# Kernel optimization log

Measured on AMD Instinct MI355X. Metric: run time of the kernel, lower is better.

The kernel has to match this reference:

```python
import jax, jax.numpy as jnp
import numpy as np

N_GRAPHS = 500
EPS = 1e-5


def setup_inputs() -> dict:
    key = jax.random.key(0)
    ks = jax.random.split(key, 10)
    N, H, OUT, E = 50000, 96, 10, 800000
    s = 1.0 / np.sqrt(H)
    x = jax.random.normal(ks[0], (N, H), jnp.float32)
    edge_index = jax.random.randint(ks[1], (2, E), 0, N, jnp.int32)
    batch = jnp.sort(jax.random.randint(ks[2], (N,), 0, N_GRAPHS, jnp.int32))
    convW = jax.random.normal(ks[3], (6, H, H), jnp.float32) * s
    convB = jnp.zeros((6, H), jnp.float32)
    bnG = jnp.ones((5, H), jnp.float32)
    bnB = jnp.zeros((5, H), jnp.float32)
    W1 = jax.random.normal(ks[4], (H, H), jnp.float32) * s
    b1 = jnp.zeros((H,), jnp.float32)
    g1 = jnp.ones((H,), jnp.float32)
    be1 = jnp.zeros((H,), jnp.float32)
    W2 = jax.random.normal(ks[5], (H, H), jnp.float32) * s
    b2 = jnp.zeros((H,), jnp.float32)
    W3 = jax.random.normal(ks[6], (H, OUT), jnp.float32) * s
    b3 = jnp.zeros((OUT,), jnp.float32)
    return dict(x=x, edge_index=edge_index, batch=batch, convW=convW, convB=convB,
                bnG=bnG, bnB=bnB, W1=W1, b1=b1, g1=g1, be1=be1, W2=W2, b2=b2, W3=W3, b3=b3)


def _batchnorm(h, g, b):
    # track_running_stats=False -> always use batch statistics (biased var)
    mu = h.mean(axis=0)
    v = jnp.mean((h - mu) ** 2, axis=0)
    return (h - mu) * jax.lax.rsqrt(v + EPS) * g + b


def reference(x, edge_index, batch, convW, convB, bnG, bnB, W1, b1, g1, be1, W2, b2, W3, b3):
    N = x.shape[0]
    src, dst = edge_index[0], edge_index[1]
    # GCN symmetric normalization with self-loops: A_hat = D^-1/2 (A+I) D^-1/2
    deg = jnp.zeros((N,), x.dtype).at[dst].add(1.0) + 1.0  # +1 for self loop
    dinv = jax.lax.rsqrt(deg)
    ew = dinv[src] * dinv[dst]            # [E] edge weights
    self_w = dinv * dinv                   # [N] self-loop weights (1/deg)

    def gcn_conv(h, W, b):
        h = h @ W
        agg = jnp.zeros_like(h).at[dst].add(ew[:, None] * h[src])
        return agg + self_w[:, None] * h + b

    # PyG BasicGNN: layers 0..4 -> conv+norm+relu+dropout; layer 5 -> conv only.
    # Dropout is identity in eval mode.
    for i in range(6):
        x = gcn_conv(x, convW[i], convB[i])
        if i < 5:
            x = jax.nn.relu(_batchnorm(x, bnG[i], bnB[i]))

    # global_mean_pool over `batch`
    cnt = jax.ops.segment_sum(jnp.ones((N,), x.dtype), batch, num_segments=N_GRAPHS)
    pooled = jax.ops.segment_sum(x, batch, num_segments=N_GRAPHS) / jnp.maximum(cnt, 1.0)[:, None]

    # prediction head: Linear -> BN -> ReLU -> (Dropout) -> Linear -> ReLU -> Linear
    h = jax.nn.relu(_batchnorm(pooled @ W1 + b1, g1, be1))
    h = jax.nn.relu(h @ W2 + b2)
    return h @ W3 + b3
```

## Files before the change

### kernel.cpp

```cpp
#include <hip/hip_runtime.h>
#include <hip/hip_fp16.h>

#define HF 96
#define C4 24
#define CH 12
#define NGRAPHS 500
#define POOL_SL 8
#define MMROWS 64
#define ATP 104
#define EPS 1e-5f

typedef _Float16 half8 __attribute__((ext_vector_type(8)));
typedef float f32x4 __attribute__((ext_vector_type(4)));

__device__ __forceinline__ float4 h4tof4(uint2 u) {
    __half2 a = *(__half2*)&u.x;
    __half2 b = *(__half2*)&u.y;
    float2 fa = __half22float2(a);
    float2 fb = __half22float2(b);
    return make_float4(fa.x, fa.y, fb.x, fb.y);
}


__global__ void count_kernel(const int* __restrict__ dst, int E, int* __restrict__ cnt) {
    int stride = gridDim.x * blockDim.x;
    for (int i = blockIdx.x * blockDim.x + threadIdx.x; i < E; i += stride)
        atomicAdd(&cnt[dst[i]], 1);
}

__global__ void node_init_kernel(const int* __restrict__ cnt, int N,
                                 float* __restrict__ dinv, float* __restrict__ selfw) {
    int stride = gridDim.x * blockDim.x;
    for (int i = blockIdx.x * blockDim.x + threadIdx.x; i < N; i += stride) {
        float d = (float)(cnt[i] + 1);
        dinv[i] = 1.0f / sqrtf(d);
        selfw[i] = 1.0f / d;
    }
}

__global__ void scan1_kernel(const int* __restrict__ cnt, int N, int* __restrict__ bsum) {
    __shared__ int s[256];
    int t = threadIdx.x;
    int i = blockIdx.x * 256 + t;
    s[t] = (i < N) ? cnt[i] : 0;
    __syncthreads();
    for (int off = 128; off; off >>= 1) {
        if (t < off) s[t] += s[t + off];
        __syncthreads();
    }
    if (t == 0) bsum[blockIdx.x] = s[0];
}

__global__ void scan2_kernel(const int* __restrict__ bsum, int NB,
                             int* __restrict__ boff, int* __restrict__ row_ptr, int N) {
    __shared__ int s[256];
    int t = threadIdx.x;
    int v = (t < NB) ? bsum[t] : 0;
    s[t] = v;
    __syncthreads();
    for (int off = 1; off < 256; off <<= 1) {
        int u = (t >= off) ? s[t - off] : 0;
        __syncthreads();
        s[t] += u;
        __syncthreads();
    }
    if (t < NB) boff[t] = s[t] - v;
    if (t == 255) row_ptr[N] = s[255];
}

__global__ void scan3_kernel(int* __restrict__ cnt, int N, const int* __restrict__ boff,
                             int* __restrict__ row_ptr) {
    __shared__ int s[256];
    int t = threadIdx.x;
    int i = blockIdx.x * 256 + t;
    int v = (i < N) ? cnt[i] : 0;
    s[t] = v;
    __syncthreads();
    for (int off = 1; off < 256; off <<= 1) {
        int u = (t >= off) ? s[t - off] : 0;
        __syncthreads();
        s[t] += u;
        __syncthreads();
    }
    if (i < N) {
        row_ptr[i] = boff[blockIdx.x] + s[t] - v;
        cnt[i] = 0;
    }
}

__global__ void scatter_kernel(const int* __restrict__ src, const int* __restrict__ dst, int E,
                               const int* __restrict__ row_ptr, int* __restrict__ cnt,
                               const float* __restrict__ dinv,
                               int2* __restrict__ csr) {
    int stride = gridDim.x * blockDim.x;
    for (int i = blockIdx.x * blockDim.x + threadIdx.x; i < E; i += stride) {
        int d = dst[i], s = src[i];
        int p = row_ptr[d] + atomicAdd(&cnt[d], 1);
        float w = dinv[s] * dinv[d];
        csr[p] = make_int2(s, __float_as_int(w));
    }
}


__global__ __launch_bounds__(256) void
matmul_kernel(const float* __restrict__ in, const float* __restrict__ W,
              _Float16* __restrict__ out, int N, int applyBN,
              const double* __restrict__ bnsum,
              const float* __restrict__ bnG, const float* __restrict__ bnB) {
    __shared__ _Float16 At[MMROWS][ATP];
    __shared__ _Float16 Wt[HF][ATP];
    __shared__ float sAl[HF], sBe[HF];
    int t = threadIdx.x;
    int n0 = blockIdx.x * MMROWS;
    int rows = N - n0; if (rows > MMROWS) rows = MMROWS;

    if (t < HF) {
        float a = 1.f, b = 0.f;
        if (applyBN) {
            double invN = 1.0 / (double)N;
            double mu = bnsum[t] * invN;
            double var = bnsum[HF + t] * invN - mu * mu;
            float v = fmaxf((float)var, 0.f) + EPS;
            a = bnG[t] / sqrtf(v);
            b = bnB[t] - (float)mu * a;
        }
        sAl[t] = a; sBe[t] = b;
    }
    __syncthreads();

#pragma unroll
    for (int j = 0; j < 6; ++j) {
        int gi = t + j * 256;
        int r = gi / C4, c4 = gi % C4;
        if (r < rows) {
            float4 v = ((const float4*)(in + (size_t)(n0 + r) * HF))[c4];
            int k = c4 * 4;
            if (applyBN) {
                v.x = fmaxf(fmaf(v.x, sAl[k + 0], sBe[k + 0]), 0.f);
                v.y = fmaxf(fmaf(v.y, sAl[k + 1], sBe[k + 1]), 0.f);
                v.z = fmaxf(fmaf(v.z, sAl[k + 2], sBe[k + 2]), 0.f);
                v.w = fmaxf(fmaf(v.w, sAl[k + 3], sBe[k + 3]), 0.f);
            }
            At[r][k + 0] = (_Float16)v.x; At[r][k + 1] = (_Float16)v.y;
            At[r][k + 2] = (_Float16)v.z; At[r][k + 3] = (_Float16)v.w;
        }
    }
#pragma unroll
    for (int j = 0; j < 9; ++j) {
        int gi = t + j * 256;
        int k = gi / C4, f4 = gi % C4;
        float4 v = ((const float4*)(W + (size_t)k * HF))[f4];
        int f = f4 * 4;
        Wt[f + 0][k] = (_Float16)v.x; Wt[f + 1][k] = (_Float16)v.y;
        Wt[f + 2][k] = (_Float16)v.z; Wt[f + 3][k] = (_Float16)v.w;
    }
    __syncthreads();

    int w = t >> 6;
    int lane = t & 63;
    int arow = w * 16 + (lane & 15);
    int k0 = (lane >> 4) * 8;
    f32x4 acc[6];
#pragma unroll
    for (int ft = 0; ft < 6; ++ft) acc[ft] = (f32x4){0.f, 0.f, 0.f, 0.f};
#pragma unroll
    for (int ks = 0; ks < 3; ++ks) {
        half8 a = *(const half8*)&At[arow][ks * 32 + k0];
#pragma unroll
        for (int ft = 0; ft < 6; ++ft) {
            half8 b = *(const half8*)&Wt[ft * 16 + (lane & 15)][ks * 32 + k0];
            acc[ft] = __builtin_amdgcn_mfma_f32_16x16x32_f16(a, b, acc[ft], 0, 0, 0);
        }
    }
    int fcol = lane & 15;
#pragma unroll
    for (int ft = 0; ft < 6; ++ft) {
#pragma unroll
        for (int j = 0; j < 4; ++j) {
            int r = w * 16 + (lane >> 4) * 4 + j;
            if (r < rows)
                out[(size_t)(n0 + r) * HF + ft * 16 + fcol] = (_Float16)acc[ft][j];
        }
    }
}


__global__ __launch_bounds__(256) void
agg_kernel(const __half* __restrict__ Hb, float* __restrict__ out,
           const int* __restrict__ row_ptr, const int2* __restrict__ csr,
           const float* __restrict__ selfw, const float* __restrict__ convB,
           int N, double* __restrict__ bnsum) {
    __shared__ float sred[2 * HF];
    bool stats = (bnsum != nullptr);
    for (int i = threadIdx.x; i < 2 * HF; i += blockDim.x) sred[i] = 0.f;
    __syncthreads();
    const uint4* h4p = (const uint4*)Hb;
    int total = N * CH;
    int stride = gridDim.x * blockDim.x;
    for (int idx = blockIdx.x * blockDim.x + threadIdx.x; idx < total; idx += stride) {
        int n = idx / CH, c = idx % CH;
        const uint4* hp = h4p + c;
        int p0 = row_ptr[n], p1 = row_ptr[n + 1];
        float sw = selfw[n];
        uint4 hraw = hp[(size_t)n * CH];
        float4 hlo = h4tof4(make_uint2(hraw.x, hraw.y));
        float4 hhi = h4tof4(make_uint2(hraw.z, hraw.w));
        float4 blo = ((const float4*)convB)[2 * c];
        float4 bhi = ((const float4*)convB)[2 * c + 1];
        float4 alo, ahi;
        alo.x = fmaf(sw, hlo.x, blo.x); alo.y = fmaf(sw, hlo.y, blo.y);
        alo.z = fmaf(sw, hlo.z, blo.z); alo.w = fmaf(sw, hlo.w, blo.w);
        ahi.x = fmaf(sw, hhi.x, bhi.x); ahi.y = fmaf(sw, hhi.y, bhi.y);
        ahi.z = fmaf(sw, hhi.z, bhi.z); ahi.w = fmaf(sw, hhi.w, bhi.w);
#define EDGE(EV, RV) { \
            float w = __int_as_float(EV.y); \
            float4 vlo = h4tof4(make_uint2(RV.x, RV.y)); \
            float4 vhi = h4tof4(make_uint2(RV.z, RV.w)); \
            alo.x = fmaf(w, vlo.x, alo.x); alo.y = fmaf(w, vlo.y, alo.y); \
            alo.z = fmaf(w, vlo.z, alo.z); alo.w = fmaf(w, vlo.w, alo.w); \
            ahi.x = fmaf(w, vhi.x, ahi.x); ahi.y = fmaf(w, vhi.y, ahi.y); \
            ahi.z = fmaf(w, vhi.z, ahi.z); ahi.w = fmaf(w, vhi.w, ahi.w); }
        int p = p0;
        for (; p + 4 <= p1; p += 4) {
            int2 e0 = csr[p], e1 = csr[p + 1], e2 = csr[p + 2], e3 = csr[p + 3];
            uint4 g0 = hp[(size_t)e0.x * CH];
            uint4 g1 = hp[(size_t)e1.x * CH];
            uint4 g2 = hp[(size_t)e2.x * CH];
            uint4 g3 = hp[(size_t)e3.x * CH];
            EDGE(e0, g0) EDGE(e1, g1) EDGE(e2, g2) EDGE(e3, g3)
        }
        for (; p < p1; ++p) {
            int2 e = csr[p];
            uint4 g = hp[(size_t)e.x * CH];
            EDGE(e, g)
        }
#undef EDGE
        ((float4*)out)[2 * idx]     = alo;
        ((float4*)out)[2 * idx + 1] = ahi;
        if (stats) {
            int f = 8 * c;
            atomicAdd(&sred[f + 0], alo.x); atomicAdd(&sred[f + 1], alo.y);
            atomicAdd(&sred[f + 2], alo.z); atomicAdd(&sred[f + 3], alo.w);
            atomicAdd(&sred[f + 4], ahi.x); atomicAdd(&sred[f + 5], ahi.y);
            atomicAdd(&sred[f + 6], ahi.z); atomicAdd(&sred[f + 7], ahi.w);
            atomicAdd(&sred[HF + f + 0], alo.x * alo.x); atomicAdd(&sred[HF + f + 1], alo.y * alo.y);
            atomicAdd(&sred[HF + f + 2], alo.z * alo.z); atomicAdd(&sred[HF + f + 3], alo.w * alo.w);
            atomicAdd(&sred[HF + f + 4], ahi.x * ahi.x); atomicAdd(&sred[HF + f + 5], ahi.y * ahi.y);
            atomicAdd(&sred[HF + f + 6], ahi.z * ahi.z); atomicAdd(&sred[HF + f + 7], ahi.w * ahi.w);
        }
    }
    if (stats) {
        __syncthreads();
        for (int i = threadIdx.x; i < 2 * HF; i += blockDim.x)
            atomicAdd(&bnsum[i], (double)sred[i]);
    }
}


__global__ __launch_bounds__(256) void
pool_kernel(const float* __restrict__ xin, const int* __restrict__ batch, int N,
            float* __restrict__ pooled) {
    int idx = blockIdx.x * blockDim.x + threadIdx.x;
    int total = NGRAPHS * POOL_SL * C4;
    if (idx >= total) return;
    int c = idx % C4;
    int q = (idx / C4) % POOL_SL;
    int g = idx / (C4 * POOL_SL);
    int lo = 0, hi = N;
    while (lo < hi) { int m = (lo + hi) >> 1; if (batch[m] < g) lo = m + 1; else hi = m; }
    int s0 = lo;
    lo = s0; hi = N;
    while (lo < hi) { int m = (lo + hi) >> 1; if (batch[m] < g + 1) lo = m + 1; else hi = m; }
    int len = lo - s0;
    int n0 = s0 + (len * q) / POOL_SL;
    int n1 = s0 + (len * (q + 1)) / POOL_SL;
    const float4* x4 = (const float4*)xin;
    float4 acc = make_float4(0.f, 0.f, 0.f, 0.f);
    for (int n = n0; n < n1; ++n) {
        float4 v0 = x4[(size_t)n * C4 + c];
        acc.x += v0.x; acc.y += v0.y; acc.z += v0.z; acc.w += v0.w;
    }
    atomicAdd(&pooled[g * HF + 4 * c + 0], acc.x);
    atomicAdd(&pooled[g * HF + 4 * c + 1], acc.y);
    atomicAdd(&pooled[g * HF + 4 * c + 2], acc.z);
    atomicAdd(&pooled[g * HF + 4 * c + 3], acc.w);
}

__global__ __launch_bounds__(128) void
head1_kernel(const float* __restrict__ pooled, const int* __restrict__ batch, int N,
             const float* __restrict__ W1, const float* __restrict__ b1,
             float* __restrict__ tmp1, double* __restrict__ bnsum) {
    __shared__ float row[HF];
    int g = blockIdx.x;
    int lo = 0, hi = N;
    while (lo < hi) { int m = (lo + hi) >> 1; if (batch[m] < g) lo = m + 1; else hi = m; }
    int s0 = lo;
    lo = s0; hi = N;
    while (lo < hi) { int m = (lo + hi) >> 1; if (batch[m] < g + 1) lo = m + 1; else hi = m; }
    int len = lo - s0;
    float inv = 1.0f / fmaxf((float)len, 1.0f);
    int f = threadIdx.x;
    if (f < HF) row[f] = pooled[g * HF + f] * inv;
    __syncthreads();
    if (f < HF) {
        float acc = b1[f];
        for (int k = 0; k < HF; ++k) acc = fmaf(row[k], W1[k * HF + f], acc);
        tmp1[g * HF + f] = acc;
        atomicAdd(&bnsum[f], (double)acc);
        atomicAdd(&bnsum[HF + f], (double)(acc * acc));
    }
}

__global__ __launch_bounds__(128) void
head23_kernel(const float* __restrict__ tmp1, const double* __restrict__ bnsum,
              const float* __restrict__ g1, const float* __restrict__ be1,
              const float* __restrict__ W2, const float* __restrict__ b2,
              const float* __restrict__ W3, const float* __restrict__ b3,
              float* __restrict__ out) {
    __shared__ float row[HF], row2[HF];
    int g = blockIdx.x;
    int f = threadIdx.x;
    if (f < HF) {
        double mu = bnsum[f] / (double)NGRAPHS;
        double var = bnsum[HF + f] / (double)NGRAPHS - mu * mu;
        float v = fmaxf((float)var, 0.f) + EPS;
        float a = g1[f] / sqrtf(v);
        float bb = be1[f] - (float)mu * a;
        row[f] = fmaxf(fmaf(tmp1[g * HF + f], a, bb), 0.f);
    }
    __syncthreads();
    if (f < HF) {
        float acc = b2[f];
        for (int k = 0; k < HF; ++k) acc = fmaf(row[k], W2[k * HF + f], acc);
        row2[f] = fmaxf(acc, 0.f);
    }
    __syncthreads();
    if (f < 10) {
        float acc = b3[f];
        for (int k = 0; k < HF; ++k) acc = fmaf(row2[k], W3[k * 10 + f], acc);
        out[g * 10 + f] = acc;
    }
}


extern "C" void kernel_launch(void* const* d_in, const int* in_sizes, int n_in,
                              void* d_out, int out_size, void* d_ws, size_t ws_size,
                              hipStream_t stream) {
    (void)n_in; (void)out_size; (void)ws_size;
    const float* x     = (const float*)d_in[0];
    const int*   ei    = (const int*)d_in[1];
    const int*   batch = (const int*)d_in[2];
    const float* convW = (const float*)d_in[3];
    const float* convB = (const float*)d_in[4];
    const float* bnG   = (const float*)d_in[5];
    const float* bnB   = (const float*)d_in[6];
    const float* W1    = (const float*)d_in[7];
    const float* b1    = (const float*)d_in[8];
    const float* g1    = (const float*)d_in[9];
    const float* be1   = (const float*)d_in[10];
    const float* W2    = (const float*)d_in[11];
    const float* b2    = (const float*)d_in[12];
    const float* W3    = (const float*)d_in[13];
    const float* b3    = (const float*)d_in[14];
    float* outp = (float*)d_out;

    int N = in_sizes[0] / HF;
    int E = in_sizes[1] / 2;
    int NB = (N + 255) / 256;
    const int* src  = ei;
    const int* dstp = ei + E;

    char* ws = (char*)d_ws;
    size_t off = 0;
    auto alloc = [&](size_t bytes) -> char* {
        char* p = ws + off;
        off += (bytes + 255) & ~(size_t)255;
        return p;
    };
    _Float16* Hb   = (_Float16*)alloc((size_t)N * HF * 2);
    float* Ob      = (float*)alloc((size_t)N * HF * 4);
    int2*  csr     = (int2*)alloc((size_t)E * 8);
    int*   row_ptr = (int*)alloc((size_t)(N + 1) * 4);
    float* dinv    = (float*)alloc((size_t)N * 4);
    float* selfw   = (float*)alloc((size_t)N * 4);
    int*   bsum    = (int*)alloc((size_t)NB * 4);
    int*   boff    = (int*)alloc((size_t)NB * 4);
    float* tmp1    = (float*)alloc((size_t)NGRAPHS * HF * 4);
    char* zstart   = ws + off;
    int*    cnt    = (int*)alloc((size_t)N * 4);
    double* bns    = (double*)alloc(6 * 2 * HF * 8);
    float*  pooled = (float*)alloc((size_t)NGRAPHS * HF * 4);
    size_t zbytes  = (size_t)((ws + off) - zstart);

    hipMemsetAsync(zstart, 0, zbytes, stream);

    count_kernel<<<1024, 256, 0, stream>>>(dstp, E, cnt);
    node_init_kernel<<<(N + 255) / 256, 256, 0, stream>>>(cnt, N, dinv, selfw);
    scan1_kernel<<<NB, 256, 0, stream>>>(cnt, N, bsum);
    scan2_kernel<<<1, 256, 0, stream>>>(bsum, NB, boff, row_ptr, N);
    scan3_kernel<<<NB, 256, 0, stream>>>(cnt, N, boff, row_ptr);
    scatter_kernel<<<1024, 256, 0, stream>>>(src, dstp, E, row_ptr, cnt, dinv, csr);

    int agg_grid = (N * CH + 255) / 256;
    int mm_grid = (N + MMROWS - 1) / MMROWS;
    const float* cur = x;
    for (int i = 0; i < 6; ++i) {
        matmul_kernel<<<mm_grid, 256, 0, stream>>>(
            cur, convW + (size_t)i * HF * HF, Hb, N,
            (i > 0) ? 1 : 0,
            (i > 0) ? bns + (size_t)(i - 1) * 2 * HF : nullptr,
            (i > 0) ? bnG + (size_t)(i - 1) * HF : nullptr,
            (i > 0) ? bnB + (size_t)(i - 1) * HF : nullptr);
        agg_kernel<<<agg_grid, 256, 0, stream>>>(
            (const __half*)Hb, Ob, row_ptr, csr, selfw,
            convB + (size_t)i * HF, N,
            (i < 5) ? bns + (size_t)i * 2 * HF : nullptr);
        cur = Ob;
    }

    int pool_grid = (NGRAPHS * POOL_SL * C4 + 255) / 256;
    pool_kernel<<<pool_grid, 256, 0, stream>>>(Ob, batch, N, pooled);
    head1_kernel<<<NGRAPHS, 128, 0, stream>>>(pooled, batch, N, W1, b1, tmp1, bns + 5 * 2 * HF);
    head23_kernel<<<NGRAPHS, 128, 0, stream>>>(tmp1, bns + 5 * 2 * HF, g1, be1, W2, b2, W3, b3, outp);
}
```

Measured before the change: 750.5 us.

## Store aggregation outputs in fp16 and fuse pooling with head layer

Aggregation now writes its output in fp16 instead of fp32, so the next matmul reads half the bytes. The matmul gains an fp16 input path that applies BN and ReLU after converting each loaded row to float. Pooling and the first head linear are merged into one per-graph kernel that reduces through shared memory, removing the global atomics. The degree/dinv init is folded into the scan3 kernel. This saves memory traffic and launches, but rounding pre-BN activations to fp16 adds precision risk, and the BN statistics are still taken from the fp32 accumulators before rounding.

```diff
diff --git a/kernel.cpp b/kernel.cpp
--- a/kernel.cpp
+++ b/kernel.cpp
@@ -5,9 +5,9 @@
 #define C4 24
 #define CH 12
 #define NGRAPHS 500
-#define POOL_SL 8
 #define MMROWS 64
 #define ATP 104
+#define PSL 20
 #define EPS 1e-5f
 
 typedef _Float16 half8 __attribute__((ext_vector_type(8)));
@@ -20,22 +20,17 @@
     float2 fb = __half22float2(b);
     return make_float4(fa.x, fa.y, fb.x, fb.y);
 }
+__device__ __forceinline__ uint2 f4toh4(float4 v) {
+    __half2 a = __floats2half2_rn(v.x, v.y);
+    __half2 b = __floats2half2_rn(v.z, v.w);
+    return make_uint2(*(unsigned int*)&a, *(unsigned int*)&b);
+}
 
 
 __global__ void count_kernel(const int* __restrict__ dst, int E, int* __restrict__ cnt) {
     int stride = gridDim.x * blockDim.x;
     for (int i = blockIdx.x * blockDim.x + threadIdx.x; i < E; i += stride)
         atomicAdd(&cnt[dst[i]], 1);
-}
-
-__global__ void node_init_kernel(const int* __restrict__ cnt, int N,
-                                 float* __restrict__ dinv, float* __restrict__ selfw) {
-    int stride = gridDim.x * blockDim.x;
-    for (int i = blockIdx.x * blockDim.x + threadIdx.x; i < N; i += stride) {
-        float d = (float)(cnt[i] + 1);
-        dinv[i] = 1.0f / sqrtf(d);
-        selfw[i] = 1.0f / d;
-    }
 }
 
 __global__ void scan1_kernel(const int* __restrict__ cnt, int N, int* __restrict__ bsum) {
@@ -69,7 +64,8 @@
 }
 
 __global__ void scan3_kernel(int* __restrict__ cnt, int N, const int* __restrict__ boff,
-                             int* __restrict__ row_ptr) {
+                             int* __restrict__ row_ptr,
+                             float* __restrict__ dinv, float* __restrict__ selfw) {
     __shared__ int s[256];
     int t = threadIdx.x;
     int i = blockIdx.x * 256 + t;
@@ -84,6 +80,9 @@
     }
     if (i < N) {
         row_ptr[i] = boff[blockIdx.x] + s[t] - v;
+        float d = (float)(v + 1);
+        dinv[i] = 1.0f / sqrtf(d);
+        selfw[i] = 1.0f / d;
         cnt[i] = 0;
     }
 }
@@ -103,8 +102,8 @@
 
 
 __global__ __launch_bounds__(256) void
-matmul_kernel(const float* __restrict__ in, const float* __restrict__ W,
-              _Float16* __restrict__ out, int N, int applyBN,
+matmul_kernel(const float* __restrict__ in32, const __half* __restrict__ inH,
+              const float* __restrict__ W, _Float16* __restrict__ out, int N, int applyBN,
               const double* __restrict__ bnsum,
               const float* __restrict__ bnG, const float* __restrict__ bnB) {
     __shared__ _Float16 At[MMROWS][ATP];
@@ -128,21 +127,45 @@
     }
     __syncthreads();
 
-#pragma unroll
-    for (int j = 0; j < 6; ++j) {
-        int gi = t + j * 256;
-        int r = gi / C4, c4 = gi % C4;
-        if (r < rows) {
-            float4 v = ((const float4*)(in + (size_t)(n0 + r) * HF))[c4];
-            int k = c4 * 4;
-            if (applyBN) {
-                v.x = fmaxf(fmaf(v.x, sAl[k + 0], sBe[k + 0]), 0.f);
-                v.y = fmaxf(fmaf(v.y, sAl[k + 1], sBe[k + 1]), 0.f);
-                v.z = fmaxf(fmaf(v.z, sAl[k + 2], sBe[k + 2]), 0.f);
-                v.w = fmaxf(fmaf(v.w, sAl[k + 3], sBe[k + 3]), 0.f);
+    if (inH) {
+#pragma unroll
+        for (int j = 0; j < 3; ++j) {
+            int gi = t + j * 256;
+            int r = gi / CH, ch = gi % CH;
+            if (r < rows) {
+                uint4 u = ((const uint4*)(inH + (size_t)(n0 + r) * HF))[ch];
+                float4 lo = h4tof4(make_uint2(u.x, u.y));
+                float4 hi = h4tof4(make_uint2(u.z, u.w));
+                int k = ch * 8;
+                if (applyBN) {
+                    lo.x = fmaxf(fmaf(lo.x, sAl[k + 0], sBe[k + 0]), 0.f);
+                    lo.y = fmaxf(fmaf(lo.y, sAl[k + 1], sBe[k + 1]), 0.f);
+                    lo.z = fmaxf(fmaf(lo.z, sAl[k + 2], sBe[k + 2]), 0.f);
+                    lo.w = fmaxf(fmaf(lo.w, sAl[k + 3], sBe[k + 3]), 0.f);
+                    hi.x = fmaxf(fmaf(hi.x, sAl[k + 4], sBe[k + 4]), 0.f);
+                    hi.y = fmaxf(fmaf(hi.y, sAl[k + 5], sBe[k + 5]), 0.f);
+                    hi.z = fmaxf(fmaf(hi.z, sAl[k + 6], sBe[k + 6]), 0.f);
+                    hi.w = fmaxf(fmaf(hi.w, sAl[k + 7], sBe[k + 7]), 0.f);
+                }
+                half8 hv;
+                hv[0] = (_Float16)lo.x; hv[1] = (_Float16)lo.y;
+                hv[2] = (_Float16)lo.z; hv[3] = (_Float16)lo.w;
+                hv[4] = (_Float16)hi.x; hv[5] = (_Float16)hi.y;
+                hv[6] = (_Float16)hi.z; hv[7] = (_Float16)hi.w;
+                *(half8*)&At[r][k] = hv;
             }
-            At[r][k + 0] = (_Float16)v.x; At[r][k + 1] = (_Float16)v.y;
-            At[r][k + 2] = (_Float16)v.z; At[r][k + 3] = (_Float16)v.w;
+        }
+    } else {
+#pragma unroll
+        for (int j = 0; j < 6; ++j) {
+            int gi = t + j * 256;
+            int r = gi / C4, c4 = gi % C4;
+            if (r < rows) {
+                float4 v = ((const float4*)(in32 + (size_t)(n0 + r) * HF))[c4];
+                int k = c4 * 4;
+                At[r][k + 0] = (_Float16)v.x; At[r][k + 1] = (_Float16)v.y;
+                At[r][k + 2] = (_Float16)v.z; At[r][k + 3] = (_Float16)v.w;
+            }
         }
     }
 #pragma unroll
@@ -186,7 +209,7 @@
 
 
 __global__ __launch_bounds__(256) void
-agg_kernel(const __half* __restrict__ Hb, float* __restrict__ out,
+agg_kernel(const __half* __restrict__ Hb, __half* __restrict__ out,
            const int* __restrict__ row_ptr, const int2* __restrict__ csr,
            const float* __restrict__ selfw, const float* __restrict__ convB,
            int N, double* __restrict__ bnsum) {
@@ -235,8 +258,8 @@
             EDGE(e, g)
         }
 #undef EDGE
-        ((float4*)out)[2 * idx]     = alo;
-        ((float4*)out)[2 * idx + 1] = ahi;
+        uint2 olo = f4toh4(alo), ohi = f4toh4(ahi);
+        ((uint4*)out)[idx] = make_uint4(olo.x, olo.y, ohi.x, ohi.y);
         if (stats) {
             int f = 8 * c;
             atomicAdd(&sred[f + 0], alo.x); atomicAdd(&sred[f + 1], alo.y);
@@ -258,56 +281,47 @@
 
 
 __global__ __launch_bounds__(256) void
-pool_kernel(const float* __restrict__ xin, const int* __restrict__ batch, int N,
-            float* __restrict__ pooled) {
-    int idx = blockIdx.x * blockDim.x + threadIdx.x;
-    int total = NGRAPHS * POOL_SL * C4;
-    if (idx >= total) return;
-    int c = idx % C4;
-    int q = (idx / C4) % POOL_SL;
-    int g = idx / (C4 * POOL_SL);
+pool_head1_kernel(const __half* __restrict__ xin, const int* __restrict__ batch, int N,
+                  const float* __restrict__ W1, const float* __restrict__ b1,
+                  float* __restrict__ tmp1, double* __restrict__ bnsum) {
+    __shared__ float sp[PSL][HF];
+    __shared__ float row[HF];
+    int g = blockIdx.x, t = threadIdx.x;
     int lo = 0, hi = N;
     while (lo < hi) { int m = (lo + hi) >> 1; if (batch[m] < g) lo = m + 1; else hi = m; }
     int s0 = lo;
     lo = s0; hi = N;
     while (lo < hi) { int m = (lo + hi) >> 1; if (batch[m] < g + 1) lo = m + 1; else hi = m; }
-    int len = lo - s0;
-    int n0 = s0 + (len * q) / POOL_SL;
-    int n1 = s0 + (len * (q + 1)) / POOL_SL;
-    const float4* x4 = (const float4*)xin;
-    float4 acc = make_float4(0.f, 0.f, 0.f, 0.f);
-    for (int n = n0; n < n1; ++n) {
-        float4 v0 = x4[(size_t)n * C4 + c];
-        acc.x += v0.x; acc.y += v0.y; acc.z += v0.z; acc.w += v0.w;
-    }
-    atomicAdd(&pooled[g * HF + 4 * c + 0], acc.x);
-    atomicAdd(&pooled[g * HF + 4 * c + 1], acc.y);
-    atomicAdd(&pooled[g * HF + 4 * c + 2], acc.z);
-    atomicAdd(&pooled[g * HF + 4 * c + 3], acc.w);
-}
-
-__global__ __launch_bounds__(128) void
-head1_kernel(const float* __restrict__ pooled, const int* __restrict__ batch, int N,
-             const float* __restrict__ W1, const float* __restrict__ b1,
-             float* __restrict__ tmp1, double* __restrict__ bnsum) {
-    __shared__ float row[HF];
-    int g = blockIdx.x;
-    int lo = 0, hi = N;
-    while (lo < hi) { int m = (lo + hi) >> 1; if (batch[m] < g) lo = m + 1; else hi = m; }
-    int s0 = lo;
-    lo = s0; hi = N;
-    while (lo < hi) { int m = (lo + hi) >> 1; if (batch[m] < g + 1) lo = m + 1; else hi = m; }
-    int len = lo - s0;
+    int s1 = lo, len = s1 - s0;
+    int c = t % CH, q = t / CH;
+    if (q < PSL) {
+        float4 aL = make_float4(0.f, 0.f, 0.f, 0.f), aH = aL;
+        for (int n = s0 + q; n < s1; n += PSL) {
+            uint4 u = ((const uint4*)(xin + (size_t)n * HF))[c];
+            float4 lo4 = h4tof4(make_uint2(u.x, u.y));
+            float4 hi4 = h4tof4(make_uint2(u.z, u.w));
+            aL.x += lo4.x; aL.y += lo4.y; aL.z += lo4.z; aL.w += lo4.w;
+            aH.x += hi4.x; aH.y += hi4.y; aH.z += hi4.z; aH.w += hi4.w;
+        }
+        int f = c * 8;
+        sp[q][f + 0] = aL.x; sp[q][f + 1] = aL.y; sp[q][f + 2] = aL.z; sp[q][f + 3] = aL.w;
+        sp[q][f + 4] = aH.x; sp[q][f + 5] = aH.y; sp[q][f + 6] = aH.z; sp[q][f + 7] = aH.w;
+    }
+    __syncthreads();
     float inv = 1.0f / fmaxf((float)len, 1.0f);
-    int f = threadIdx.x;
-    if (f < HF) row[f] = pooled[g * HF + f] * inv;
-    __syncthreads();
-    if (f < HF) {
-        float acc = b1[f];
-        for (int k = 0; k < HF; ++k) acc = fmaf(row[k], W1[k * HF + f], acc);
-        tmp1[g * HF + f] = acc;
-        atomicAdd(&bnsum[f], (double)acc);
-        atomicAdd(&bnsum[HF + f], (double)(acc * acc));
+    if (t < HF) {
+        float s = 0.f;
+#pragma unroll
+        for (int q2 = 0; q2 < PSL; ++q2) s += sp[q2][t];
+        row[t] = s * inv;
+    }
+    __syncthreads();
+    if (t < HF) {
+        float acc = b1[t];
+        for (int k = 0; k < HF; ++k) acc = fmaf(row[k], W1[k * HF + t], acc);
+        tmp1[g * HF + t] = acc;
+        atomicAdd(&bnsum[t], (double)acc);
+        atomicAdd(&bnsum[HF + t], (double)(acc * acc));
     }
 }
 
@@ -378,7 +392,7 @@
         return p;
     };
     _Float16* Hb   = (_Float16*)alloc((size_t)N * HF * 2);
-    float* Ob      = (float*)alloc((size_t)N * HF * 4);
+    _Float16* Ob   = (_Float16*)alloc((size_t)N * HF * 2);
     int2*  csr     = (int2*)alloc((size_t)E * 8);
     int*   row_ptr = (int*)alloc((size_t)(N + 1) * 4);
     float* dinv    = (float*)alloc((size_t)N * 4);
@@ -389,37 +403,34 @@
     char* zstart   = ws + off;
     int*    cnt    = (int*)alloc((size_t)N * 4);
     double* bns    = (double*)alloc(6 * 2 * HF * 8);
-    float*  pooled = (float*)alloc((size_t)NGRAPHS * HF * 4);
     size_t zbytes  = (size_t)((ws + off) - zstart);
 
     hipMemsetAsync(zstart, 0, zbytes, stream);
 
     count_kernel<<<1024, 256, 0, stream>>>(dstp, E, cnt);
-    node_init_kernel<<<(N + 255) / 256, 256, 0, stream>>>(cnt, N, dinv, selfw);
     scan1_kernel<<<NB, 256, 0, stream>>>(cnt, N, bsum);
     scan2_kernel<<<1, 256, 0, stream>>>(bsum, NB, boff, row_ptr, N);
-    scan3_kernel<<<NB, 256, 0, stream>>>(cnt, N, boff, row_ptr);
+    scan3_kernel<<<NB, 256, 0, stream>>>(cnt, N, boff, row_ptr, dinv, selfw);
     scatter_kernel<<<1024, 256, 0, stream>>>(src, dstp, E, row_ptr, cnt, dinv, csr);
 
     int agg_grid = (N * CH + 255) / 256;
     int mm_grid = (N + MMROWS - 1) / MMROWS;
-    const float* cur = x;
     for (int i = 0; i < 6; ++i) {
         matmul_kernel<<<mm_grid, 256, 0, stream>>>(
-            cur, convW + (size_t)i * HF * HF, Hb, N,
+            (i == 0) ? x : nullptr,
+            (i == 0) ? nullptr : (const __half*)Ob,
+            convW + (size_t)i * HF * HF, Hb, N,
             (i > 0) ? 1 : 0,
             (i > 0) ? bns + (size_t)(i - 1) * 2 * HF : nullptr,
             (i > 0) ? bnG + (size_t)(i - 1) * HF : nullptr,
             (i > 0) ? bnB + (size_t)(i - 1) * HF : nullptr);
         agg_kernel<<<agg_grid, 256, 0, stream>>>(
-            (const __half*)Hb, Ob, row_ptr, csr, selfw,
+            (const __half*)Hb, (__half*)Ob, row_ptr, csr, selfw,
             convB + (size_t)i * HF, N,
             (i < 5) ? bns + (size_t)i * 2 * HF : nullptr);
-        cur = Ob;
-    }
-
-    int pool_grid = (NGRAPHS * POOL_SL * C4 + 255) / 256;
-    pool_kernel<<<pool_grid, 256, 0, stream>>>(Ob, batch, N, pooled);
-    head1_kernel<<<NGRAPHS, 128, 0, stream>>>(pooled, batch, N, W1, b1, tmp1, bns + 5 * 2 * HF);
+    }
+
+    pool_head1_kernel<<<NGRAPHS, 256, 0, stream>>>((const __half*)Ob, batch, N,
+                                                   W1, b1, tmp1, bns + 5 * 2 * HF);
     head23_kernel<<<NGRAPHS, 128, 0, stream>>>(tmp1, bns + 5 * 2 * HF, g1, be1, W2, b2, W3, b3, outp);
 }
```

Measured after the change: 725.3 us. -3.4%, faster.
